# Kernel optimization log

Hardware: AMD Instinct MI355X
Metric: run time of the kernel (lower is better)

## Reference

```python
import jax, jax.numpy as jnp
import numpy as np

NUM_EMBEDDINGS = 256
EMBEDDING_DIM = 128
NUM_LAYERS = 2


def setup_inputs() -> dict:
    key = jax.random.key(0)
    k1, k2 = jax.random.split(key)
    x = jax.random.normal(k1, (8, 65536, EMBEDDING_DIM), dtype=jnp.float32)
    codebooks = jax.random.normal(
        k2, (NUM_LAYERS, NUM_EMBEDDINGS, EMBEDDING_DIM), dtype=jnp.float32)
    return {"x": x, "codebooks": codebooks}


def _quantize_layer(residual, codebook):
    # residual: [B, N, D]; codebook: [K, D]
    # squared L2 distances without materializing differences:
    # ||r||^2 - 2 r.c + ||c||^2  -> [B, N, K]
    r2 = jnp.sum(residual * residual, axis=-1, keepdims=True)      # [B,N,1]
    c2 = jnp.sum(codebook * codebook, axis=-1)                     # [K]
    dots = jnp.einsum("bnd,kd->bnk", residual, codebook)           # [B,N,K]
    dists = r2 - 2.0 * dots + c2                                   # [B,N,K]
    indices = jnp.argmin(dists, axis=-1)                           # [B,N] int
    quantized = jnp.take(codebook, indices, axis=0)                # [B,N,D]
    return quantized, indices


def reference(x, codebooks):
    """Residual VQ: cdist + argmin + lookup across NUM_LAYERS layers.

    Returns (quantized_out_with_straight_through, indices [L,B,N]).
    """
    residual = x
    quantized_out = jnp.zeros_like(x)
    all_indices = []
    for l in range(NUM_LAYERS):
        q, idx = _quantize_layer(residual, codebooks[l])
        residual = residual - q
        quantized_out = quantized_out + q
        all_indices.append(idx)
    # straight-through estimator (standard VQ forward)
    quantized_st = x + jax.lax.stop_gradient(quantized_out - x)
    return quantized_st, jnp.stack(all_indices, axis=0)
```

## Files before the change

### kernel.cpp

```cpp
#include <hip/hip_runtime.h>
#include <hip/hip_fp16.h>
#include <math.h>

#define DDIM    128
#define KCODES  256
#define NTOKS   (8 * 65536)
#define TAUKEY  62914
#define CTAU    0.01f

typedef float f32x4 __attribute__((ext_vector_type(4)));
typedef _Float16 half8 __attribute__((ext_vector_type(8)));

#define MFMAH(a, b, c) __builtin_amdgcn_mfma_f32_16x16x32_f16(a, b, c, 0, 0, 0)

union H8 { uint4 u; half8 h; };

__device__ __forceinline__ half8 pk4(float a0, float a1, float a2, float a3,
                                     float b0, float b1, float b2, float b3) {
    H8 r;
    r.u.x = __builtin_bit_cast(unsigned, __builtin_amdgcn_cvt_pkrtz(a0, a1));
    r.u.y = __builtin_bit_cast(unsigned, __builtin_amdgcn_cvt_pkrtz(a2, a3));
    r.u.z = __builtin_bit_cast(unsigned, __builtin_amdgcn_cvt_pkrtz(b0, b1));
    r.u.w = __builtin_bit_cast(unsigned, __builtin_amdgcn_cvt_pkrtz(b2, b3));
    return r.h;
}

__device__ __forceinline__ void split8(const float4& A, const float4& B,
                                       half8& hi, half8& lo) {
    hi = pk4(A.x, A.y, A.z, A.w, B.x, B.y, B.z, B.w);
    lo = pk4(A.x - (float)hi[0], A.y - (float)hi[1],
             A.z - (float)hi[2], A.w - (float)hi[3],
             B.x - (float)hi[4], B.y - (float)hi[5],
             B.z - (float)hi[6], B.w - (float)hi[7]);
}

__global__ __attribute__((amdgpu_waves_per_eu(2, 2))) __launch_bounds__(512)
void rvq_screen14(
    const float* __restrict__ x, const float* __restrict__ cb,
    float* __restrict__ out, unsigned* __restrict__ ws, unsigned wcap)
{
    __shared__ __align__(16) _Float16 chs[2 * KCODES * DDIM];
    __shared__ float kc2[2 * KCODES];
    __shared__ int   bidx[8][2][32];

    const int tid   = threadIdx.x;
    const int w     = tid >> 6;
    const int lane  = tid & 63;
    const int lquad = lane >> 4;
    const int l15   = lane & 15;

    float4 pfx[2][4][2];

#define XLOAD(T) do {                                                          \
        const size_t bb_ = (size_t)blockIdx.x * 2048 + (size_t)(T) * 256 +     \
                           (size_t)w * 32;                                     \
        _Pragma("unroll")                                                      \
        for (int mt_ = 0; mt_ < 2; ++mt_) {                                    \
            const float* xp_ = x + (bb_ + (size_t)(mt_ * 16 + l15)) * DDIM +   \
                               lquad * 8;                                      \
            _Pragma("unroll")                                                  \
            for (int k_ = 0; k_ < 4; ++k_) {                                   \
                pfx[mt_][k_][0] = *(const float4*)(xp_ + k_ * 32);             \
                pfx[mt_][k_][1] = *(const float4*)(xp_ + k_ * 32 + 4);         \
            }                                                                  \
        }                                                                      \
    } while (0)

    XLOAD(0);

    #pragma unroll
    for (int ph = 0; ph < 4; ++ph) {
        const int row = ph * 128 + (tid >> 2);
        const int sq  = tid & 3;
        const int code = row & 255;
        const float* src = cb + (size_t)row * DDIM + sq * 32;
        float c2p = 0.f;
        #pragma unroll
        for (int s = 0; s < 4; ++s) {
            const float4 a = ((const float4*)src)[s * 2 + 0];
            const float4 b = ((const float4*)src)[s * 2 + 1];
            half8 hh;
            hh[0] = (_Float16)a.x; hh[1] = (_Float16)a.y;
            hh[2] = (_Float16)a.z; hh[3] = (_Float16)a.w;
            hh[4] = (_Float16)b.x; hh[5] = (_Float16)b.y;
            hh[6] = (_Float16)b.z; hh[7] = (_Float16)b.w;
            c2p = fmaf(a.x, a.x, c2p); c2p = fmaf(a.y, a.y, c2p);
            c2p = fmaf(a.z, a.z, c2p); c2p = fmaf(a.w, a.w, c2p);
            c2p = fmaf(b.x, b.x, c2p); c2p = fmaf(b.y, b.y, c2p);
            c2p = fmaf(b.z, b.z, c2p); c2p = fmaf(b.w, b.w, c2p);
            const unsigned c = (unsigned)(sq * 4 + s);
            const unsigned off = ((unsigned)(row >> 8) << 16) + (unsigned)code * 256u +
                                 ((c ^ ((unsigned)code & 15u)) << 4);
            *(half8*)((char*)chs + off) = hh;
        }
        c2p += __shfl_xor(c2p, 1);
        c2p += __shfl_xor(c2p, 2);
        if (sq == 0) kc2[row] = c2p * 8192.0f;
    }
    __syncthreads();

    #pragma unroll 1
    for (int t = 0; t < 8; ++t) {
        const size_t base = (size_t)blockIdx.x * 2048 + (size_t)t * 256 + (size_t)w * 32;

        half8 ah[2][4], al[2][4];
        #pragma unroll
        for (int mt = 0; mt < 2; ++mt)
            #pragma unroll
            for (int kst = 0; kst < 4; ++kst)
                split8(pfx[mt][kst][0], pfx[mt][kst][1], ah[mt][kst], al[mt][kst]);

        XLOAD(t < 7 ? t + 1 : 7);

        #pragma unroll
        for (int l = 0; l < 2; ++l) {
            int b1[2][4], b2[2][4];
            #pragma unroll
            for (int mt = 0; mt < 2; ++mt)
                #pragma unroll
                for (int rg = 0; rg < 4; ++rg) { b1[mt][rg] = 0x7FFFFFFF; b2[mt][rg] = 0x7FFFFFFF; }

            #pragma unroll
            for (int cg = 0; cg < 16; ++cg) {
                f32x4 acc0 = (f32x4){0.f, 0.f, 0.f, 0.f};
                f32x4 acc1 = (f32x4){0.f, 0.f, 0.f, 0.f};
                const unsigned codeL = (unsigned)(cg * 16 + l15);
                #pragma unroll
                for (int kst = 0; kst < 4; ++kst) {
                    const unsigned off = ((unsigned)l << 16) + codeL * 256u +
                        ((((unsigned)(kst * 4 + lquad)) ^ (codeL & 15u)) << 4);
                    const half8 bh = *(half8*)((char*)chs + off);
                    acc0 = MFMAH(ah[0][kst], bh, acc0);
                    acc0 = MFMAH(al[0][kst], bh, acc0);
                    acc1 = MFMAH(ah[1][kst], bh, acc1);
                    acc1 = MFMAH(al[1][kst], bh, acc1);
                }
                const int codeg = cg * 16 + l15;
                const float kc = kc2[l * KCODES + codeg];
                #pragma unroll
                for (int mt = 0; mt < 2; ++mt) {
                    const f32x4& acc = mt ? acc1 : acc0;
                    #pragma unroll
                    for (int rg = 0; rg < 4; ++rg) {
                        const float dk = fmaf(-16384.f, acc[rg], kc);
                        const int key = ((int)dk << 8) + codeg;
                        const int mx = (b1[mt][rg] > key) ? b1[mt][rg] : key;
                        b1[mt][rg] = (b1[mt][rg] < key) ? b1[mt][rg] : key;
                        b2[mt][rg] = (b2[mt][rg] < mx) ? b2[mt][rg] : mx;
                    }
                }
            }

            #pragma unroll
            for (int m = 1; m <= 8; m <<= 1) {
                #pragma unroll
                for (int mt = 0; mt < 2; ++mt)
                    #pragma unroll
                    for (int rg = 0; rg < 4; ++rg) {
                        const int ob1 = __shfl_xor(b1[mt][rg], m);
                        const int ob2 = __shfl_xor(b2[mt][rg], m);
                        const int mx = (b1[mt][rg] > ob1) ? b1[mt][rg] : ob1;
                        const int mn2 = (b2[mt][rg] < ob2) ? b2[mt][rg] : ob2;
                        b1[mt][rg] = (b1[mt][rg] < ob1) ? b1[mt][rg] : ob1;
                        b2[mt][rg] = (mn2 < mx) ? mn2 : mx;
                    }
            }

            if (l15 == 0) {
                #pragma unroll
                for (int mt = 0; mt < 2; ++mt)
                    #pragma unroll
                    for (int rg = 0; rg < 4; ++rg) {
                        const int trel = mt * 16 + lquad * 4 + rg;
                        const int code = b1[mt][rg] & 0xFF;
                        bidx[w][l][trel] = code;
                        out[(size_t)NTOKS * DDIM + (size_t)l * NTOKS + base + trel] = (float)code;
                        if ((long long)b2[mt][rg] - (long long)b1[mt][rg] < (long long)TAUKEY) {
                            const unsigned p = atomicAdd(ws, 1u);
                            if (p < wcap) ws[8 + p] = (unsigned)(base + trel);
                        }
                    }
            }

            if (l == 0) {
                #pragma unroll
                for (int mt = 0; mt < 2; ++mt) {
                    const int b0 = bidx[w][0][mt * 16 + l15];
                    const float* c0p = cb + (size_t)b0 * DDIM;
                    #pragma unroll
                    for (int kst = 0; kst < 4; ++kst) {
                        const float4 ca = *(const float4*)(c0p + kst * 32 + lquad * 8);
                        const float4 cbv = *(const float4*)(c0p + kst * 32 + lquad * 8 + 4);
                        const half8 h = ah[mt][kst], lo = al[mt][kst];
                        float4 d0, d1;
                        d0.x = ((float)h[0] + (float)lo[0]) - ca.x;
                        d0.y = ((float)h[1] + (float)lo[1]) - ca.y;
                        d0.z = ((float)h[2] + (float)lo[2]) - ca.z;
                        d0.w = ((float)h[3] + (float)lo[3]) - ca.w;
                        d1.x = ((float)h[4] + (float)lo[4]) - cbv.x;
                        d1.y = ((float)h[5] + (float)lo[5]) - cbv.y;
                        d1.z = ((float)h[6] + (float)lo[6]) - cbv.z;
                        d1.w = ((float)h[7] + (float)lo[7]) - cbv.w;
                        split8(d0, d1, ah[mt][kst], al[mt][kst]);
                    }
                }
            }
        }

        #pragma unroll
        for (int mt = 0; mt < 2; ++mt) {
            const int trel = mt * 16 + l15;
            const int b0e = bidx[w][0][trel];
            const int b1e = bidx[w][1][trel];
            const float* p0 = cb + (size_t)b0e * DDIM;
            const float* p1 = cb + ((size_t)KCODES + b1e) * DDIM;
            float* op = out + (base + (size_t)trel) * DDIM;
            #pragma unroll
            for (int kst = 0; kst < 4; ++kst) {
                const float4 a0 = *(const float4*)(p0 + kst * 32 + lquad * 8);
                const float4 a1 = *(const float4*)(p0 + kst * 32 + lquad * 8 + 4);
                const float4 z0 = *(const float4*)(p1 + kst * 32 + lquad * 8);
                const float4 z1 = *(const float4*)(p1 + kst * 32 + lquad * 8 + 4);
                const float4 o0 = {a0.x + z0.x, a0.y + z0.y, a0.z + z0.z, a0.w + z0.w};
                const float4 o1 = {a1.x + z1.x, a1.y + z1.y, a1.z + z1.z, a1.w + z1.w};
                *(float4*)(op + kst * 32 + lquad * 8)     = o0;
                *(float4*)(op + kst * 32 + lquad * 8 + 4) = o1;
            }
        }
    }
#undef XLOAD
}

__global__ __launch_bounds__(256, 4) void rvq_rescue2(
    const float* __restrict__ x, const float* __restrict__ cb,
    float* __restrict__ out, const unsigned* __restrict__ ws, unsigned wcap)
{
    __shared__ float rshF[4][DDIM];
    const int tid = threadIdx.x, lane = tid & 63, w = tid >> 6;

    unsigned cnt = ws[0]; if (cnt > wcap) cnt = wcap;
    const unsigned nwaves = gridDim.x * 4;

    for (unsigned wi = blockIdx.x * 4 + w; wi < cnt; wi += nwaves) {
        const size_t tok = ws[8 + wi];
        const float* xrow = x + tok * DDIM;
        const float x0 = xrow[lane], x1 = xrow[lane + 64];
        double rd0 = (double)x0, rd1 = (double)x1;
        rshF[w][lane] = x0; rshF[w][lane + 64] = x1;

        #pragma unroll
        for (int l = 0; l < 2; ++l) {
            const float* cbl = cb + (size_t)l * KCODES * DDIM;

            float d32[4];
            #pragma unroll
            for (int cc = 0; cc < 4; ++cc) {
                const float* crow = cbl + (size_t)(lane * 4 + cc) * DDIM;
                float s0 = 0.f, s1 = 0.f, s2 = 0.f, s3 = 0.f;
                #pragma unroll 8
                for (int i = 0; i < DDIM; i += 4) {
                    const float e0 = rshF[w][i + 0] - crow[i + 0];
                    const float e1 = rshF[w][i + 1] - crow[i + 1];
                    const float e2 = rshF[w][i + 2] - crow[i + 2];
                    const float e3 = rshF[w][i + 3] - crow[i + 3];
                    s0 = fmaf(e0, e0, s0); s1 = fmaf(e1, e1, s1);
                    s2 = fmaf(e2, e2, s2); s3 = fmaf(e3, e3, s3);
                }
                d32[cc] = (s0 + s1) + (s2 + s3);
            }
            float wmin = fminf(fminf(d32[0], d32[1]), fminf(d32[2], d32[3]));
            #pragma unroll
            for (int m = 1; m < 64; m <<= 1) wmin = fminf(wmin, __shfl_xor(wmin, m));

            double bestd = 1e300; int bestc = 0x7FFFFFFF;
            #pragma unroll
            for (int cc = 0; cc < 4; ++cc) {
                unsigned long long msk = __ballot(d32[cc] <= wmin + CTAU);
                while (msk) {
                    const int ln = __ffsll((long long)msk) - 1; msk &= msk - 1;
                    const int code = ln * 4 + cc;
                    const float* crow = cbl + (size_t)code * DDIM;
                    const double e0 = rd0 - (double)crow[lane];
                    const double e1 = rd1 - (double)crow[lane + 64];
                    double v = fma(e0, e0, e1 * e1);
                    #pragma unroll
                    for (int m = 1; m < 64; m <<= 1) v += __shfl_xor(v, m);
                    if (v < bestd || (v == bestd && code < bestc)) { bestd = v; bestc = code; }
                }
            }

            const float* qrow = cbl + (size_t)bestc * DDIM;
            rd0 -= (double)qrow[lane];
            rd1 -= (double)qrow[lane + 64];
            if (l == 0) { rshF[w][lane] = (float)rd0; rshF[w][lane + 64] = (float)rd1; }
            if (lane == 0)
                out[(size_t)NTOKS * DDIM + (size_t)l * NTOKS + tok] = (float)bestc;
        }

        float* orow = out + tok * DDIM;
        orow[lane]      = (float)((double)x0 - rd0);
        orow[lane + 64] = (float)((double)x1 - rd1);
    }
}

extern "C" void kernel_launch(void* const* d_in, const int* in_sizes, int n_in,
                              void* d_out, int out_size, void* d_ws, size_t ws_size,
                              hipStream_t stream) {
    const float* x  = (const float*)d_in[0];
    const float* cb = (const float*)d_in[1];
    float* out = (float*)d_out;
    unsigned* ws = (unsigned*)d_ws;
    unsigned wcap = (ws_size >= 64) ? (unsigned)(ws_size / 4 - 16) : 0;

    hipMemsetAsync(d_ws, 0, 4, stream);
    hipLaunchKernelGGL(rvq_screen14, dim3(256), dim3(512), 0, stream,
                       x, cb, out, ws, wcap);
    hipLaunchKernelGGL(rvq_rescue2, dim3(2048), dim3(256), 0, stream,
                       x, cb, out, ws, wcap);
}
```

Baseline: 473.4 us.

## Split fused two-layer screen kernel into separate per-layer kernels

Replaces the single kernel that handled both RVQ layers per block with two kernels, one per layer, each holding only that layer's fp16 codebook in shared memory (half the LDS) and launched on 512 blocks of 1024 tokens each. The second kernel rereads x and the layer-0 index from the output buffer, rebuilds the residual, and writes the summed codes. This lowers LDS use and register pressure so more blocks fit per CU and the grid fills the device better. In exchange x is read twice from HBM, the indices take an extra round trip through global memory, and there is one more kernel launch.

```diff
diff --git a/kernel.cpp b/kernel.cpp
--- a/kernel.cpp
+++ b/kernel.cpp
@@ -34,14 +34,13 @@
              B.z - (float)hi[6], B.w - (float)hi[7]);
 }
 
-__global__ __attribute__((amdgpu_waves_per_eu(2, 2))) __launch_bounds__(512)
-void rvq_screen14(
+
+__global__ __launch_bounds__(512) void rvq_l0(
     const float* __restrict__ x, const float* __restrict__ cb,
     float* __restrict__ out, unsigned* __restrict__ ws, unsigned wcap)
 {
-    __shared__ __align__(16) _Float16 chs[2 * KCODES * DDIM];
-    __shared__ float kc2[2 * KCODES];
-    __shared__ int   bidx[8][2][32];
+    __shared__ __align__(16) _Float16 chs[KCODES * DDIM];
+    __shared__ float kc2[KCODES];
 
     const int tid   = threadIdx.x;
     const int w     = tid >> 6;
@@ -52,7 +51,7 @@
     float4 pfx[2][4][2];
 
 #define XLOAD(T) do {                                                          \
-        const size_t bb_ = (size_t)blockIdx.x * 2048 + (size_t)(T) * 256 +     \
+        const size_t bb_ = (size_t)blockIdx.x * 1024 + (size_t)(T) * 256 +     \
                            (size_t)w * 32;                                     \
         _Pragma("unroll")                                                      \
         for (int mt_ = 0; mt_ < 2; ++mt_) {                                    \
@@ -69,11 +68,10 @@
     XLOAD(0);
 
     #pragma unroll
-    for (int ph = 0; ph < 4; ++ph) {
-        const int row = ph * 128 + (tid >> 2);
+    for (int ph = 0; ph < 2; ++ph) {
+        const int code = ph * 128 + (tid >> 2);
         const int sq  = tid & 3;
-        const int code = row & 255;
-        const float* src = cb + (size_t)row * DDIM + sq * 32;
+        const float* src = cb + (size_t)code * DDIM + sq * 32;
         float c2p = 0.f;
         #pragma unroll
         for (int s = 0; s < 4; ++s) {
@@ -89,19 +87,19 @@
             c2p = fmaf(b.x, b.x, c2p); c2p = fmaf(b.y, b.y, c2p);
             c2p = fmaf(b.z, b.z, c2p); c2p = fmaf(b.w, b.w, c2p);
             const unsigned c = (unsigned)(sq * 4 + s);
-            const unsigned off = ((unsigned)(row >> 8) << 16) + (unsigned)code * 256u +
+            const unsigned off = (unsigned)code * 256u +
                                  ((c ^ ((unsigned)code & 15u)) << 4);
             *(half8*)((char*)chs + off) = hh;
         }
         c2p += __shfl_xor(c2p, 1);
         c2p += __shfl_xor(c2p, 2);
-        if (sq == 0) kc2[row] = c2p * 8192.0f;
+        if (sq == 0) kc2[code] = c2p * 8192.0f;
     }
     __syncthreads();
 
     #pragma unroll 1
-    for (int t = 0; t < 8; ++t) {
-        const size_t base = (size_t)blockIdx.x * 2048 + (size_t)t * 256 + (size_t)w * 32;
+    for (int t = 0; t < 4; ++t) {
+        const size_t base = (size_t)blockIdx.x * 1024 + (size_t)t * 256 + (size_t)w * 32;
 
         half8 ah[2][4], al[2][4];
         #pragma unroll
@@ -110,125 +108,244 @@
             for (int kst = 0; kst < 4; ++kst)
                 split8(pfx[mt][kst][0], pfx[mt][kst][1], ah[mt][kst], al[mt][kst]);
 
-        XLOAD(t < 7 ? t + 1 : 7);
-
-        #pragma unroll
-        for (int l = 0; l < 2; ++l) {
-            int b1[2][4], b2[2][4];
+        XLOAD(t < 3 ? t + 1 : 3);
+
+        int b1[2][4], b2[2][4];
+        #pragma unroll
+        for (int mt = 0; mt < 2; ++mt)
+            #pragma unroll
+            for (int rg = 0; rg < 4; ++rg) { b1[mt][rg] = 0x7FFFFFFF; b2[mt][rg] = 0x7FFFFFFF; }
+
+        #pragma unroll
+        for (int cg = 0; cg < 16; ++cg) {
+            f32x4 acc0 = (f32x4){0.f, 0.f, 0.f, 0.f};
+            f32x4 acc1 = (f32x4){0.f, 0.f, 0.f, 0.f};
+            const unsigned codeL = (unsigned)(cg * 16 + l15);
+            #pragma unroll
+            for (int kst = 0; kst < 4; ++kst) {
+                const unsigned off = codeL * 256u +
+                    ((((unsigned)(kst * 4 + lquad)) ^ (codeL & 15u)) << 4);
+                const half8 bh = *(half8*)((char*)chs + off);
+                acc0 = MFMAH(ah[0][kst], bh, acc0);
+                acc0 = MFMAH(al[0][kst], bh, acc0);
+                acc1 = MFMAH(ah[1][kst], bh, acc1);
+                acc1 = MFMAH(al[1][kst], bh, acc1);
+            }
+            const int codeg = cg * 16 + l15;
+            const float kc = kc2[codeg];
+            #pragma unroll
+            for (int mt = 0; mt < 2; ++mt) {
+                const f32x4& acc = mt ? acc1 : acc0;
+                #pragma unroll
+                for (int rg = 0; rg < 4; ++rg) {
+                    const float dk = fmaf(-16384.f, acc[rg], kc);
+                    const int key = ((int)dk << 8) + codeg;
+                    const int mx = (b1[mt][rg] > key) ? b1[mt][rg] : key;
+                    b1[mt][rg] = (b1[mt][rg] < key) ? b1[mt][rg] : key;
+                    b2[mt][rg] = (b2[mt][rg] < mx) ? b2[mt][rg] : mx;
+                }
+            }
+        }
+
+        #pragma unroll
+        for (int m = 1; m <= 8; m <<= 1) {
             #pragma unroll
             for (int mt = 0; mt < 2; ++mt)
                 #pragma unroll
-                for (int rg = 0; rg < 4; ++rg) { b1[mt][rg] = 0x7FFFFFFF; b2[mt][rg] = 0x7FFFFFFF; }
-
-            #pragma unroll
-            for (int cg = 0; cg < 16; ++cg) {
-                f32x4 acc0 = (f32x4){0.f, 0.f, 0.f, 0.f};
-                f32x4 acc1 = (f32x4){0.f, 0.f, 0.f, 0.f};
-                const unsigned codeL = (unsigned)(cg * 16 + l15);
-                #pragma unroll
-                for (int kst = 0; kst < 4; ++kst) {
-                    const unsigned off = ((unsigned)l << 16) + codeL * 256u +
-                        ((((unsigned)(kst * 4 + lquad)) ^ (codeL & 15u)) << 4);
-                    const half8 bh = *(half8*)((char*)chs + off);
-                    acc0 = MFMAH(ah[0][kst], bh, acc0);
-                    acc0 = MFMAH(al[0][kst], bh, acc0);
-                    acc1 = MFMAH(ah[1][kst], bh, acc1);
-                    acc1 = MFMAH(al[1][kst], bh, acc1);
-                }
-                const int codeg = cg * 16 + l15;
-                const float kc = kc2[l * KCODES + codeg];
-                #pragma unroll
-                for (int mt = 0; mt < 2; ++mt) {
-                    const f32x4& acc = mt ? acc1 : acc0;
-                    #pragma unroll
-                    for (int rg = 0; rg < 4; ++rg) {
-                        const float dk = fmaf(-16384.f, acc[rg], kc);
-                        const int key = ((int)dk << 8) + codeg;
-                        const int mx = (b1[mt][rg] > key) ? b1[mt][rg] : key;
-                        b1[mt][rg] = (b1[mt][rg] < key) ? b1[mt][rg] : key;
-                        b2[mt][rg] = (b2[mt][rg] < mx) ? b2[mt][rg] : mx;
+                for (int rg = 0; rg < 4; ++rg) {
+                    const int ob1 = __shfl_xor(b1[mt][rg], m);
+                    const int ob2 = __shfl_xor(b2[mt][rg], m);
+                    const int mx = (b1[mt][rg] > ob1) ? b1[mt][rg] : ob1;
+                    const int mn2 = (b2[mt][rg] < ob2) ? b2[mt][rg] : ob2;
+                    b1[mt][rg] = (b1[mt][rg] < ob1) ? b1[mt][rg] : ob1;
+                    b2[mt][rg] = (mn2 < mx) ? mn2 : mx;
+                }
+        }
+
+        if (l15 == 0) {
+            #pragma unroll
+            for (int mt = 0; mt < 2; ++mt)
+                #pragma unroll
+                for (int rg = 0; rg < 4; ++rg) {
+                    const int trel = mt * 16 + lquad * 4 + rg;
+                    const int code = b1[mt][rg] & 0xFF;
+                    out[(size_t)NTOKS * DDIM + base + trel] = (float)code;
+                    if ((long long)b2[mt][rg] - (long long)b1[mt][rg] < (long long)TAUKEY) {
+                        const unsigned p = atomicAdd(ws, 1u);
+                        if (p < wcap) ws[8 + p] = (unsigned)(base + trel);
                     }
                 }
-            }
-
-            #pragma unroll
-            for (int m = 1; m <= 8; m <<= 1) {
-                #pragma unroll
-                for (int mt = 0; mt < 2; ++mt)
-                    #pragma unroll
-                    for (int rg = 0; rg < 4; ++rg) {
-                        const int ob1 = __shfl_xor(b1[mt][rg], m);
-                        const int ob2 = __shfl_xor(b2[mt][rg], m);
-                        const int mx = (b1[mt][rg] > ob1) ? b1[mt][rg] : ob1;
-                        const int mn2 = (b2[mt][rg] < ob2) ? b2[mt][rg] : ob2;
-                        b1[mt][rg] = (b1[mt][rg] < ob1) ? b1[mt][rg] : ob1;
-                        b2[mt][rg] = (mn2 < mx) ? mn2 : mx;
+        }
+    }
+#undef XLOAD
+}
+
+__global__ __launch_bounds__(512) void rvq_l1(
+    const float* __restrict__ x, const float* __restrict__ cb,
+    float* __restrict__ out, unsigned* __restrict__ ws, unsigned wcap)
+{
+    __shared__ __align__(16) _Float16 chs[KCODES * DDIM];
+    __shared__ float kc2[KCODES];
+    __shared__ int   bidx[8][32];
+
+    const int tid   = threadIdx.x;
+    const int w     = tid >> 6;
+    const int lane  = tid & 63;
+    const int lquad = lane >> 4;
+    const int l15   = lane & 15;
+
+    #pragma unroll
+    for (int ph = 0; ph < 2; ++ph) {
+        const int code = ph * 128 + (tid >> 2);
+        const int sq  = tid & 3;
+        const float* src = cb + (size_t)(KCODES + code) * DDIM + sq * 32;
+        float c2p = 0.f;
+        #pragma unroll
+        for (int s = 0; s < 4; ++s) {
+            const float4 a = ((const float4*)src)[s * 2 + 0];
+            const float4 b = ((const float4*)src)[s * 2 + 1];
+            half8 hh;
+            hh[0] = (_Float16)a.x; hh[1] = (_Float16)a.y;
+            hh[2] = (_Float16)a.z; hh[3] = (_Float16)a.w;
+            hh[4] = (_Float16)b.x; hh[5] = (_Float16)b.y;
+            hh[6] = (_Float16)b.z; hh[7] = (_Float16)b.w;
+            c2p = fmaf(a.x, a.x, c2p); c2p = fmaf(a.y, a.y, c2p);
+            c2p = fmaf(a.z, a.z, c2p); c2p = fmaf(a.w, a.w, c2p);
+            c2p = fmaf(b.x, b.x, c2p); c2p = fmaf(b.y, b.y, c2p);
+            c2p = fmaf(b.z, b.z, c2p); c2p = fmaf(b.w, b.w, c2p);
+            const unsigned c = (unsigned)(sq * 4 + s);
+            const unsigned off = (unsigned)code * 256u +
+                                 ((c ^ ((unsigned)code & 15u)) << 4);
+            *(half8*)((char*)chs + off) = hh;
+        }
+        c2p += __shfl_xor(c2p, 1);
+        c2p += __shfl_xor(c2p, 2);
+        if (sq == 0) kc2[code] = c2p * 8192.0f;
+    }
+    __syncthreads();
+
+    #pragma unroll 1
+    for (int t = 0; t < 4; ++t) {
+        const size_t base = (size_t)blockIdx.x * 1024 + (size_t)t * 256 + (size_t)w * 32;
+
+        int b0[2];
+        #pragma unroll
+        for (int mt = 0; mt < 2; ++mt)
+            b0[mt] = (int)out[(size_t)NTOKS * DDIM + base + (size_t)(mt * 16 + l15)];
+
+        float4 c0s[2][4][2];
+        half8 ah[2][4], al[2][4];
+        #pragma unroll
+        for (int mt = 0; mt < 2; ++mt) {
+            const float* xp = x + (base + (size_t)(mt * 16 + l15)) * DDIM + lquad * 8;
+            const float* cp = cb + (size_t)b0[mt] * DDIM + lquad * 8;
+            #pragma unroll
+            for (int kst = 0; kst < 4; ++kst) {
+                const float4 xa = *(const float4*)(xp + kst * 32);
+                const float4 xb = *(const float4*)(xp + kst * 32 + 4);
+                c0s[mt][kst][0] = *(const float4*)(cp + kst * 32);
+                c0s[mt][kst][1] = *(const float4*)(cp + kst * 32 + 4);
+                float4 d0, d1;
+                d0.x = xa.x - c0s[mt][kst][0].x;
+                d0.y = xa.y - c0s[mt][kst][0].y;
+                d0.z = xa.z - c0s[mt][kst][0].z;
+                d0.w = xa.w - c0s[mt][kst][0].w;
+                d1.x = xb.x - c0s[mt][kst][1].x;
+                d1.y = xb.y - c0s[mt][kst][1].y;
+                d1.z = xb.z - c0s[mt][kst][1].z;
+                d1.w = xb.w - c0s[mt][kst][1].w;
+                split8(d0, d1, ah[mt][kst], al[mt][kst]);
+            }
+        }
+
+        int b1[2][4], b2[2][4];
+        #pragma unroll
+        for (int mt = 0; mt < 2; ++mt)
+            #pragma unroll
+            for (int rg = 0; rg < 4; ++rg) { b1[mt][rg] = 0x7FFFFFFF; b2[mt][rg] = 0x7FFFFFFF; }
+
+        #pragma unroll
+        for (int cg = 0; cg < 16; ++cg) {
+            f32x4 acc0 = (f32x4){0.f, 0.f, 0.f, 0.f};
+            f32x4 acc1 = (f32x4){0.f, 0.f, 0.f, 0.f};
+            const unsigned codeL = (unsigned)(cg * 16 + l15);
+            #pragma unroll
+            for (int kst = 0; kst < 4; ++kst) {
+                const unsigned off = codeL * 256u +
+                    ((((unsigned)(kst * 4 + lquad)) ^ (codeL & 15u)) << 4);
+                const half8 bh = *(half8*)((char*)chs + off);
+                acc0 = MFMAH(ah[0][kst], bh, acc0);
+                acc0 = MFMAH(al[0][kst], bh, acc0);
+                acc1 = MFMAH(ah[1][kst], bh, acc1);
+                acc1 = MFMAH(al[1][kst], bh, acc1);
+            }
+            const int codeg = cg * 16 + l15;
+            const float kc = kc2[codeg];
+            #pragma unroll
+            for (int mt = 0; mt < 2; ++mt) {
+                const f32x4& acc = mt ? acc1 : acc0;
+                #pragma unroll
+                for (int rg = 0; rg < 4; ++rg) {
+                    const float dk = fmaf(-16384.f, acc[rg], kc);
+                    const int key = ((int)dk << 8) + codeg;
+                    const int mx = (b1[mt][rg] > key) ? b1[mt][rg] : key;
+                    b1[mt][rg] = (b1[mt][rg] < key) ? b1[mt][rg] : key;
+                    b2[mt][rg] = (b2[mt][rg] < mx) ? b2[mt][rg] : mx;
+                }
+            }
+        }
+
+        #pragma unroll
+        for (int m = 1; m <= 8; m <<= 1) {
+            #pragma unroll
+            for (int mt = 0; mt < 2; ++mt)
+                #pragma unroll
+                for (int rg = 0; rg < 4; ++rg) {
+                    const int ob1 = __shfl_xor(b1[mt][rg], m);
+                    const int ob2 = __shfl_xor(b2[mt][rg], m);
+                    const int mx = (b1[mt][rg] > ob1) ? b1[mt][rg] : ob1;
+                    const int mn2 = (b2[mt][rg] < ob2) ? b2[mt][rg] : ob2;
+                    b1[mt][rg] = (b1[mt][rg] < ob1) ? b1[mt][rg] : ob1;
+                    b2[mt][rg] = (mn2 < mx) ? mn2 : mx;
+                }
+        }
+
+        if (l15 == 0) {
+            #pragma unroll
+            for (int mt = 0; mt < 2; ++mt)
+                #pragma unroll
+                for (int rg = 0; rg < 4; ++rg) {
+                    const int trel = mt * 16 + lquad * 4 + rg;
+                    const int code = b1[mt][rg] & 0xFF;
+                    bidx[w][trel] = code;
+                    out[(size_t)NTOKS * DDIM + (size_t)NTOKS + base + trel] = (float)code;
+                    if ((long long)b2[mt][rg] - (long long)b1[mt][rg] < (long long)TAUKEY) {
+                        const unsigned p = atomicAdd(ws, 1u);
+                        if (p < wcap) ws[8 + p] = (unsigned)(base + trel);
                     }
-            }
-
-            if (l15 == 0) {
-                #pragma unroll
-                for (int mt = 0; mt < 2; ++mt)
-                    #pragma unroll
-                    for (int rg = 0; rg < 4; ++rg) {
-                        const int trel = mt * 16 + lquad * 4 + rg;
-                        const int code = b1[mt][rg] & 0xFF;
-                        bidx[w][l][trel] = code;
-                        out[(size_t)NTOKS * DDIM + (size_t)l * NTOKS + base + trel] = (float)code;
-                        if ((long long)b2[mt][rg] - (long long)b1[mt][rg] < (long long)TAUKEY) {
-                            const unsigned p = atomicAdd(ws, 1u);
-                            if (p < wcap) ws[8 + p] = (unsigned)(base + trel);
-                        }
-                    }
-            }
-
-            if (l == 0) {
-                #pragma unroll
-                for (int mt = 0; mt < 2; ++mt) {
-                    const int b0 = bidx[w][0][mt * 16 + l15];
-                    const float* c0p = cb + (size_t)b0 * DDIM;
-                    #pragma unroll
-                    for (int kst = 0; kst < 4; ++kst) {
-                        const float4 ca = *(const float4*)(c0p + kst * 32 + lquad * 8);
-                        const float4 cbv = *(const float4*)(c0p + kst * 32 + lquad * 8 + 4);
-                        const half8 h = ah[mt][kst], lo = al[mt][kst];
-                        float4 d0, d1;
-                        d0.x = ((float)h[0] + (float)lo[0]) - ca.x;
-                        d0.y = ((float)h[1] + (float)lo[1]) - ca.y;
-                        d0.z = ((float)h[2] + (float)lo[2]) - ca.z;
-                        d0.w = ((float)h[3] + (float)lo[3]) - ca.w;
-                        d1.x = ((float)h[4] + (float)lo[4]) - cbv.x;
-                        d1.y = ((float)h[5] + (float)lo[5]) - cbv.y;
-                        d1.z = ((float)h[6] + (float)lo[6]) - cbv.z;
-                        d1.w = ((float)h[7] + (float)lo[7]) - cbv.w;
-                        split8(d0, d1, ah[mt][kst], al[mt][kst]);
-                    }
-                }
-            }
+                }
         }
 
         #pragma unroll
         for (int mt = 0; mt < 2; ++mt) {
             const int trel = mt * 16 + l15;
-            const int b0e = bidx[w][0][trel];
-            const int b1e = bidx[w][1][trel];
-            const float* p0 = cb + (size_t)b0e * DDIM;
-            const float* p1 = cb + ((size_t)KCODES + b1e) * DDIM;
-            float* op = out + (base + (size_t)trel) * DDIM;
+            const int b1e = bidx[w][trel];
+            const float* p1 = cb + ((size_t)KCODES + b1e) * DDIM + lquad * 8;
+            float* op = out + (base + (size_t)trel) * DDIM + lquad * 8;
             #pragma unroll
             for (int kst = 0; kst < 4; ++kst) {
-                const float4 a0 = *(const float4*)(p0 + kst * 32 + lquad * 8);
-                const float4 a1 = *(const float4*)(p0 + kst * 32 + lquad * 8 + 4);
-                const float4 z0 = *(const float4*)(p1 + kst * 32 + lquad * 8);
-                const float4 z1 = *(const float4*)(p1 + kst * 32 + lquad * 8 + 4);
-                const float4 o0 = {a0.x + z0.x, a0.y + z0.y, a0.z + z0.z, a0.w + z0.w};
-                const float4 o1 = {a1.x + z1.x, a1.y + z1.y, a1.z + z1.z, a1.w + z1.w};
-                *(float4*)(op + kst * 32 + lquad * 8)     = o0;
-                *(float4*)(op + kst * 32 + lquad * 8 + 4) = o1;
+                const float4 z0 = *(const float4*)(p1 + kst * 32);
+                const float4 z1 = *(const float4*)(p1 + kst * 32 + 4);
+                float4 o0, o1;
+                o0.x = c0s[mt][kst][0].x + z0.x; o0.y = c0s[mt][kst][0].y + z0.y;
+                o0.z = c0s[mt][kst][0].z + z0.z; o0.w = c0s[mt][kst][0].w + z0.w;
+                o1.x = c0s[mt][kst][1].x + z1.x; o1.y = c0s[mt][kst][1].y + z1.y;
+                o1.z = c0s[mt][kst][1].z + z1.z; o1.w = c0s[mt][kst][1].w + z1.w;
+                *(float4*)(op + kst * 32)     = o0;
+                *(float4*)(op + kst * 32 + 4) = o1;
             }
         }
     }
-#undef XLOAD
 }
 
 __global__ __launch_bounds__(256, 4) void rvq_rescue2(
@@ -313,7 +430,9 @@
     unsigned wcap = (ws_size >= 64) ? (unsigned)(ws_size / 4 - 16) : 0;
 
     hipMemsetAsync(d_ws, 0, 4, stream);
-    hipLaunchKernelGGL(rvq_screen14, dim3(256), dim3(512), 0, stream,
+    hipLaunchKernelGGL(rvq_l0, dim3(512), dim3(512), 0, stream,
+                       x, cb, out, ws, wcap);
+    hipLaunchKernelGGL(rvq_l1, dim3(512), dim3(512), 0, stream,
                        x, cb, out, ws, wcap);
     hipLaunchKernelGGL(rvq_rescue2, dim3(2048), dim3(256), 0, stream,
                        x, cb, out, ws, wcap);
```

Measured after the change: 717.6 us. 51.6% more time.
